# Performance work log

Measured on AMD Instinct MI355X. Metric: run time of the kernel, lower is better.

## Reference

```python
import jax, jax.numpy as jnp
import numpy as np

T, B, D, H = 512, 64, 512, 512

def setup_inputs() -> dict:
    key = jax.random.key(0)
    ks = jax.random.split(key, 12)
    s_in = 1.0 / np.sqrt(D + H)
    s_res = 1.0 / np.sqrt(D)
    inp = {
        'inputs': jax.random.normal(ks[0], (T, B, D), jnp.float32),
        'W_f': jax.random.uniform(ks[1], (H, D + H), jnp.float32, -s_in, s_in),
        'b_f': jax.random.uniform(ks[2], (H,), jnp.float32, -s_in, s_in),
        'W_i': jax.random.uniform(ks[3], (H, D + H), jnp.float32, -s_in, s_in),
        'b_i': jax.random.uniform(ks[4], (H,), jnp.float32, -s_in, s_in),
        'W_g': jax.random.uniform(ks[5], (H, D + H), jnp.float32, -s_in, s_in),
        'b_g': jax.random.uniform(ks[6], (H,), jnp.float32, -s_in, s_in),
        'W_o': jax.random.uniform(ks[7], (H, D + H), jnp.float32, -s_in, s_in),
        'b_o': jax.random.uniform(ks[8], (H,), jnp.float32, -s_in, s_in),
        'W_r': jax.random.uniform(ks[9], (H, D), jnp.float32, -s_res, s_res),
        'b_r': jax.random.uniform(ks[10], (H,), jnp.float32, -s_res, s_res),
    }
    return inp

def reference(inputs, W_f, b_f, W_i, b_i, W_g, b_g, W_o, b_o, W_r, b_r):
    Bsz = inputs.shape[1]
    Hd = W_f.shape[0]
    # residual projection is independent of recurrence: batch it over all timesteps
    res = jnp.einsum('tbd,hd->tbh', inputs, W_r) + b_r  # [T,B,H]

    def step(carry, xr):
        hx, cx = carry
        x, r = xr
        combined = jnp.concatenate([x, hx], axis=1)  # [B, D+H]
        f = jax.nn.sigmoid(combined @ W_f.T + b_f)
        i = jax.nn.sigmoid(combined @ W_i.T + b_i)
        g = jnp.tanh(combined @ W_g.T + b_g)
        o = jax.nn.sigmoid(combined @ W_o.T + b_o)
        cx = f * cx + i * g
        hx = o * jnp.tanh(cx) + r  # use_residual=True
        return (hx, cx), hx

    hx0 = jnp.zeros((Bsz, Hd), inputs.dtype)
    cx0 = jnp.zeros((Bsz, Hd), inputs.dtype)
    (hx, cx), stacked = jax.lax.scan(step, (hx0, cx0), (inputs, res))
    return stacked, (hx, cx)
```

## Files before the change

kernel.cpp:

```cpp
#include <hip/hip_runtime.h>


typedef __bf16         bfrag8 __attribute__((ext_vector_type(8)));
typedef float          f32x4v __attribute__((ext_vector_type(4)));
typedef unsigned short u16x8  __attribute__((ext_vector_type(8)));
typedef int            v4i    __attribute__((ext_vector_type(4)));

#define N_TB    32768
#define GXW     2560
#define OUT_HX  16777216
#define OUT_CX  16809984

__device__ __forceinline__ float bf2f(unsigned short u) {
  unsigned int x = ((unsigned int)u) << 16;
  return __builtin_bit_cast(float, x);
}
__device__ __forceinline__ unsigned short f2bf(float f) {
  unsigned int x = __builtin_bit_cast(unsigned int, f);
  x = x + 0x7FFFu + ((x >> 16) & 1u);
  return (unsigned short)(x >> 16);
}
__device__ __forceinline__ float sigf(float x) {
  x = fminf(fmaxf(x, -30.f), 30.f);
  return 1.f / (1.f + __expf(-x));
}
__device__ __forceinline__ float tanh_f(float x) {
  x = fminf(fmaxf(x, -15.f), 15.f);
  float e = __expf(-2.f * x);
  return (1.f - e) / (1.f + e);
}

__global__ void cvt_kernel(const float* __restrict__ in, unsigned short* __restrict__ out) {
  int i = (blockIdx.x * 256 + threadIdx.x) * 4;
  float4 v = *(const float4*)(in + i);
  ushort4 o = make_ushort4(f2bf(v.x), f2bf(v.y), f2bf(v.z), f2bf(v.w));
  *(ushort4*)(out + i) = o;
}

__global__ void repack_kernel(const float* __restrict__ Wf, const float* __restrict__ Wi,
                              const float* __restrict__ Wg, const float* __restrict__ Wo,
                              const float* __restrict__ Wr,
                              const float* __restrict__ bfp, const float* __restrict__ bip,
                              const float* __restrict__ bgp, const float* __restrict__ bop,
                              const float* __restrict__ brp,
                              unsigned short* __restrict__ Wc, unsigned short* __restrict__ Whx,
                              float* __restrict__ bias) {
  int tid = blockIdx.x * 256 + threadIdx.x;
  if (tid < 262144) {
    int row = tid >> 7;
    int k4  = (tid & 127) * 4;
    int g = row >> 9, h = row & 511;
    const float* W = (g == 0) ? Wf : (g == 1) ? Wi : (g == 2) ? Wg : Wo;
    float4 a = *(const float4*)(W + (size_t)h * 1024 + k4);
    float4 b = *(const float4*)(W + (size_t)h * 1024 + 512 + k4);
    *(ushort4*)(Wc  + (size_t)row * 512 + k4) = make_ushort4(f2bf(a.x), f2bf(a.y), f2bf(a.z), f2bf(a.w));
    *(ushort4*)(Whx + (size_t)row * 512 + k4) = make_ushort4(f2bf(b.x), f2bf(b.y), f2bf(b.z), f2bf(b.w));
  } else if (tid < 327680) {
    int t2 = tid - 262144;
    int row = t2 >> 7;
    int k4  = (t2 & 127) * 4;
    float4 a = *(const float4*)(Wr + (size_t)row * 512 + k4);
    *(ushort4*)(Wc + (size_t)(2048 + row) * 512 + k4) =
        make_ushort4(f2bf(a.x), f2bf(a.y), f2bf(a.z), f2bf(a.w));
  }
  if (tid < 2560) {
    float v;
    if      (tid <  512) v = bfp[tid];
    else if (tid < 1024) v = bip[tid - 512];
    else if (tid < 1536) v = bgp[tid - 1024];
    else if (tid < 2048) v = bop[tid - 1536];
    else                 v = brp[tid - 2048];
    bias[tid] = v;
  }
}

__global__ __launch_bounds__(256)
void gemm_kernel(const unsigned short* __restrict__ A, const unsigned short* __restrict__ B,
                 const float* __restrict__ bias, unsigned short* __restrict__ C) {
  const int bm = blockIdx.x;
  const int bn = blockIdx.y;
  const int tid = threadIdx.x;
  const int lane = tid & 63;
  const int w = tid >> 6;
  const int wm = w & 1, wn = w >> 1;
  const int col = lane & 15, q = lane >> 4;

  __shared__ unsigned short As[128 * 64] __attribute__((aligned(16)));
  __shared__ unsigned short Bs[128 * 64] __attribute__((aligned(16)));

  f32x4v acc[4][4] = {};

  for (int kt = 0; kt < 8; ++kt) {
    __syncthreads();
    #pragma unroll
    for (int p = 0; p < 4; ++p) {
      int idx = p * 256 + tid;
      int row = idx >> 3, gc = idx & 7;
      *(u16x8*)(&As[idx * 8]) = *(const u16x8*)(A + (size_t)(bm * 128 + row) * 512 + kt * 64 + gc * 8);
      *(u16x8*)(&Bs[idx * 8]) = *(const u16x8*)(B + (size_t)(bn * 128 + row) * 512 + kt * 64 + gc * 8);
    }
    __syncthreads();
    #pragma unroll
    for (int kk = 0; kk < 2; ++kk) {
      bfrag8 af[4], bfr[4];
      #pragma unroll
      for (int mt = 0; mt < 4; ++mt)
        af[mt] = *(const bfrag8*)(&As[(wm * 64 + mt * 16 + col) * 64 + kk * 32 + q * 8]);
      #pragma unroll
      for (int nt = 0; nt < 4; ++nt)
        bfr[nt] = *(const bfrag8*)(&Bs[(wn * 64 + nt * 16 + col) * 64 + kk * 32 + q * 8]);
      #pragma unroll
      for (int mt = 0; mt < 4; ++mt)
        #pragma unroll
        for (int nt = 0; nt < 4; ++nt)
          acc[mt][nt] = __builtin_amdgcn_mfma_f32_16x16x32_bf16(af[mt], bfr[nt], acc[mt][nt], 0, 0, 0);
    }
  }
  #pragma unroll
  for (int mt = 0; mt < 4; ++mt) {
    const int m0 = bm * 128 + wm * 64 + mt * 16 + q * 4;
    const float4 b4 = *(const float4*)(bias + m0);
    #pragma unroll
    for (int nt = 0; nt < 4; ++nt) {
      const int n = bn * 128 + wn * 64 + nt * 16 + col;
      f32x4v v = acc[mt][nt];
      ushort4 o = make_ushort4(f2bf(v[0] + b4.x), f2bf(v[1] + b4.y),
                               f2bf(v[2] + b4.z), f2bf(v[3] + b4.w));
      *(ushort4*)(C + (size_t)n * GXW + m0) = o;
    }
  }
}

__global__ __launch_bounds__(256, 1)
void recur_kernel(const unsigned short* __restrict__ Whx, const unsigned short* __restrict__ gx,
                  unsigned short* __restrict__ hbuf, int* flags, float* __restrict__ out) {
  const int jb = blockIdx.x;
  const int tid = threadIdx.x;
  const int lane = tid & 63;
  const int w = tid >> 6;
  const int gp = w & 1;
  const int mh = w >> 1;
  const int col = lane & 15;
  const int q = lane >> 4;

  __shared__ float S[4][64][20] __attribute__((aligned(16)));
  __shared__ unsigned short Hs[64][520] __attribute__((aligned(16)));

  bfrag8 Bf[2][16];
  #pragma unroll
  for (int g2 = 0; g2 < 2; ++g2) {
    const int gate = gp * 2 + g2;
    const unsigned short* wp = Whx + (size_t)(gate * 512 + jb * 16 + col) * 512 + q * 8;
    #pragma unroll
    for (int kk = 0; kk < 16; ++kk)
      Bf[g2][kk] = *(const bfrag8*)(wp + kk * 32);
  }

  const int ub = tid >> 2;
  const int ucg = (tid & 3) * 4;
  float c4[4] = {0.f, 0.f, 0.f, 0.f};

  ushort4 gxv[4], rv;
  {
    const unsigned short* g0 = gx + (size_t)ub * GXW + jb * 16 + ucg;
    #pragma unroll
    for (int gg = 0; gg < 4; ++gg) gxv[gg] = *(const ushort4*)(g0 + gg * 512);
    rv = *(const ushort4*)(g0 + 2048);
  }

  for (int t = 0; t < 512; ++t) {
    if (t > 0) {
      if (tid < 32) {
        while (__hip_atomic_load(flags + tid, __ATOMIC_RELAXED, __HIP_MEMORY_SCOPE_AGENT) < t) {
        }
      }
      __syncthreads();
    }

    {
      const char* hsrc = (const char*)(hbuf + (t & 1) * 32768);
      v4i tmp[16];
      #pragma unroll
      for (int i = 0; i < 16; ++i) {
        const char* p = hsrc + (size_t)(i * 256 + tid) * 16;
        asm volatile("global_load_dwordx4 %0, %1, off sc0 sc1"
                     : "=v"(tmp[i]) : "v"(p) : "memory");
      }
      asm volatile("s_waitcnt vmcnt(0)" ::: "memory");
      #pragma unroll
      for (int i = 0; i < 16; ++i) {
        int idx = i * 256 + tid;
        *(v4i*)((char*)&Hs[0][0] + (size_t)(idx >> 6) * 1040 + (idx & 63) * 16) = tmp[i];
      }
    }
    __syncthreads();

    bfrag8 Af[2][16];
    #pragma unroll
    for (int mt = 0; mt < 2; ++mt) {
      const unsigned short* ap = &Hs[mh * 32 + mt * 16 + col][q * 8];
      #pragma unroll
      for (int kk = 0; kk < 16; ++kk)
        Af[mt][kk] = *(const bfrag8*)(ap + kk * 32);
    }
    f32x4v acc[2][2] = {};
    #pragma unroll
    for (int kk = 0; kk < 16; ++kk)
      #pragma unroll
      for (int mt = 0; mt < 2; ++mt)
        #pragma unroll
        for (int g2 = 0; g2 < 2; ++g2)
          acc[mt][g2] = __builtin_amdgcn_mfma_f32_16x16x32_bf16(Af[mt][kk], Bf[g2][kk], acc[mt][g2], 0, 0, 0);

    #pragma unroll
    for (int mt = 0; mt < 2; ++mt)
      #pragma unroll
      for (int g2 = 0; g2 < 2; ++g2) {
        const int gate = gp * 2 + g2;
        const int b0 = mh * 32 + mt * 16 + q * 4;
        #pragma unroll
        for (int r = 0; r < 4; ++r)
          S[gate][b0 + r][col] = acc[mt][g2][r];
      }
    __syncthreads();

    float pre[4][4];
    #pragma unroll
    for (int gg = 0; gg < 4; ++gg) {
      float4 sv = *(const float4*)&S[gg][ub][ucg];
      pre[gg][0] = sv.x + bf2f(gxv[gg].x);
      pre[gg][1] = sv.y + bf2f(gxv[gg].y);
      pre[gg][2] = sv.z + bf2f(gxv[gg].z);
      pre[gg][3] = sv.w + bf2f(gxv[gg].w);
    }
    float rres[4] = {bf2f(rv.x), bf2f(rv.y), bf2f(rv.z), bf2f(rv.w)};
    float hv[4];
    #pragma unroll
    for (int j = 0; j < 4; ++j) {
      float fg = sigf(pre[0][j]);
      float ig = sigf(pre[1][j]);
      float gg = tanh_f(pre[2][j]);
      float og = sigf(pre[3][j]);
      c4[j] = fg * c4[j] + ig * gg;
      hv[j] = og * tanh_f(c4[j]) + rres[j];
    }
    float4 h4 = make_float4(hv[0], hv[1], hv[2], hv[3]);

    if (t < 511) {
      ushort4 hb4 = make_ushort4(f2bf(hv[0]), f2bf(hv[1]), f2bf(hv[2]), f2bf(hv[3]));
      union { ushort4 u4; unsigned long long u64; } pk;
      pk.u4 = hb4;
      __hip_atomic_store((unsigned long long*)(hbuf + ((t + 1) & 1) * 32768 + ub * 512 + jb * 16 + ucg),
                         pk.u64, __ATOMIC_RELAXED, __HIP_MEMORY_SCOPE_AGENT);
      asm volatile("s_waitcnt vmcnt(0)" ::: "memory");
      __syncthreads();
      if (tid == 0)
        __hip_atomic_store(flags + jb, t + 1, __ATOMIC_RELAXED, __HIP_MEMORY_SCOPE_AGENT);
    }

    *(float4*)(out + (size_t)t * 32768 + ub * 512 + jb * 16 + ucg) = h4;

    if (t == 511) {
      *(float4*)(out + OUT_HX + ub * 512 + jb * 16 + ucg) = h4;
      *(float4*)(out + OUT_CX + ub * 512 + jb * 16 + ucg) = make_float4(c4[0], c4[1], c4[2], c4[3]);
    } else {
      const unsigned short* gn = gx + (size_t)((t + 1) * 64 + ub) * GXW + jb * 16 + ucg;
      #pragma unroll
      for (int gg = 0; gg < 4; ++gg) gxv[gg] = *(const ushort4*)(gn + gg * 512);
      rv = *(const ushort4*)(gn + 2048);
    }
  }
}

extern "C" void kernel_launch(void* const* d_in, const int* in_sizes, int n_in,
                              void* d_out, int out_size, void* d_ws, size_t ws_size,
                              hipStream_t stream) {
  const float* inputs = (const float*)d_in[0];
  const float* Wf = (const float*)d_in[1];
  const float* bf_ = (const float*)d_in[2];
  const float* Wi = (const float*)d_in[3];
  const float* bi_ = (const float*)d_in[4];
  const float* Wg = (const float*)d_in[5];
  const float* bg_ = (const float*)d_in[6];
  const float* Wo = (const float*)d_in[7];
  const float* bo_ = (const float*)d_in[8];
  const float* Wr = (const float*)d_in[9];
  const float* br_ = (const float*)d_in[10];
  float* out = (float*)d_out;

  unsigned short* X    = (unsigned short*)d_ws;
  unsigned short* Wc   = X + 16777216;
  unsigned short* Whx  = Wc + 1310720;
  float*          bias = (float*)(Whx + 1048576);
  unsigned short* gx   = (unsigned short*)(bias + 2560);
  unsigned short* hbuf = gx + 83886080;
  int*            flags = (int*)(hbuf + 65536);
  const size_t ws_needed = 206186624;
  if (ws_size < ws_needed) return;

  hipMemsetAsync(hbuf, 0, 65536 * 2 + 32 * 4, stream);

  cvt_kernel<<<16384, 256, 0, stream>>>(inputs, X);
  repack_kernel<<<1280, 256, 0, stream>>>(Wf, Wi, Wg, Wo, Wr, bf_, bi_, bg_, bo_, br_,
                                          Wc, Whx, bias);
  gemm_kernel<<<dim3(20, 256), 256, 0, stream>>>(Wc, X, bias, gx);
  recur_kernel<<<32, 256, 0, stream>>>(Whx, gx, hbuf, flags, out);
}
```

Baseline: 2.498 ms.

## Replace flag-based grid sync with per-element tagged h buffer and 512 threads

```diff
diff --git a/kernel.cpp b/kernel.cpp
--- a/kernel.cpp
+++ b/kernel.cpp
@@ -5,6 +5,7 @@
 typedef float          f32x4v __attribute__((ext_vector_type(4)));
 typedef unsigned short u16x8  __attribute__((ext_vector_type(8)));
 typedef int            v4i    __attribute__((ext_vector_type(4)));
+typedef int            v2i    __attribute__((ext_vector_type(2)));
 
 #define N_TB    32768
 #define GXW     2560
@@ -131,9 +132,9 @@
   }
 }
 
-__global__ __launch_bounds__(256, 1)
+__global__ __launch_bounds__(512, 1)
 void recur_kernel(const unsigned short* __restrict__ Whx, const unsigned short* __restrict__ gx,
-                  unsigned short* __restrict__ hbuf, int* flags, float* __restrict__ out) {
+                  unsigned int* __restrict__ hbufF, float* __restrict__ out) {
   const int jb = blockIdx.x;
   const int tid = threadIdx.x;
   const int lane = tid & 63;
@@ -156,118 +157,119 @@
       Bf[g2][kk] = *(const bfrag8*)(wp + kk * 32);
   }
 
-  const int ub = tid >> 2;
-  const int ucg = (tid & 3) * 4;
-  float c4[4] = {0.f, 0.f, 0.f, 0.f};
-
-  ushort4 gxv[4], rv;
+  const int ub = tid >> 3;
+  const int uc = (tid & 7) * 2;
+
+  float c2[2] = {0.f, 0.f};
+
+  ushort2 gxv[4], rv;
   {
-    const unsigned short* g0 = gx + (size_t)ub * GXW + jb * 16 + ucg;
-    #pragma unroll
-    for (int gg = 0; gg < 4; ++gg) gxv[gg] = *(const ushort4*)(g0 + gg * 512);
-    rv = *(const ushort4*)(g0 + 2048);
+    const unsigned short* g0 = gx + (size_t)ub * GXW + jb * 16 + uc;
+    #pragma unroll
+    for (int gg = 0; gg < 4; ++gg) gxv[gg] = *(const ushort2*)(g0 + gg * 512);
+    rv = *(const ushort2*)(g0 + 2048);
   }
 
   for (int t = 0; t < 512; ++t) {
-    if (t > 0) {
-      if (tid < 32) {
-        while (__hip_atomic_load(flags + tid, __ATOMIC_RELAXED, __HIP_MEMORY_SCOPE_AGENT) < t) {
+    {
+      const char* hs = (const char*)(hbufF + (t & 1) * 32768);
+      v4i ta[8], tb_[8];
+      const int need = (t > 0);
+      for (;;) {
+        #pragma unroll
+        for (int i = 0; i < 8; ++i) {
+          const char* p = hs + (size_t)(i * 512 + tid) * 32;
+          asm volatile("global_load_dwordx4 %0, %1, off sc0 sc1"
+                       : "=v"(ta[i]) : "v"(p) : "memory");
+          asm volatile("global_load_dwordx4 %0, %1, off sc0 sc1"
+                       : "=v"(tb_[i]) : "v"(p + 16) : "memory");
         }
+        asm volatile("s_waitcnt vmcnt(0)" ::: "memory");
+        if (!need) break;
+        unsigned int bad = 0;
+        #pragma unroll
+        for (int i = 0; i < 8; ++i)
+          #pragma unroll
+          for (int j = 0; j < 4; ++j) {
+            bad |= (unsigned int)(ta[i][j]  ^ t) & 0xFFFFu;
+            bad |= (unsigned int)(tb_[i][j] ^ t) & 0xFFFFu;
+          }
+        if (!bad) break;
       }
-      __syncthreads();
-    }
-
+      #pragma unroll
+      for (int i = 0; i < 8; ++i) {
+        const int u = i * 512 + tid;
+        v4i o;
+        o[0] = (int)(((unsigned int)ta[i][0]  >> 16) | ((unsigned int)ta[i][1]  & 0xFFFF0000u));
+        o[1] = (int)(((unsigned int)ta[i][2]  >> 16) | ((unsigned int)ta[i][3]  & 0xFFFF0000u));
+        o[2] = (int)(((unsigned int)tb_[i][0] >> 16) | ((unsigned int)tb_[i][1] & 0xFFFF0000u));
+        o[3] = (int)(((unsigned int)tb_[i][2] >> 16) | ((unsigned int)tb_[i][3] & 0xFFFF0000u));
+        *(v4i*)((char*)&Hs[0][0] + (size_t)(u >> 6) * 1040 + (u & 63) * 16) = o;
+      }
+    }
+    __syncthreads();
+
+    bfrag8 Af[16];
     {
-      const char* hsrc = (const char*)(hbuf + (t & 1) * 32768);
-      v4i tmp[16];
-      #pragma unroll
-      for (int i = 0; i < 16; ++i) {
-        const char* p = hsrc + (size_t)(i * 256 + tid) * 16;
-        asm volatile("global_load_dwordx4 %0, %1, off sc0 sc1"
-                     : "=v"(tmp[i]) : "v"(p) : "memory");
-      }
-      asm volatile("s_waitcnt vmcnt(0)" ::: "memory");
-      #pragma unroll
-      for (int i = 0; i < 16; ++i) {
-        int idx = i * 256 + tid;
-        *(v4i*)((char*)&Hs[0][0] + (size_t)(idx >> 6) * 1040 + (idx & 63) * 16) = tmp[i];
-      }
+      const unsigned short* ap = &Hs[mh * 16 + col][q * 8];
+      #pragma unroll
+      for (int kk = 0; kk < 16; ++kk)
+        Af[kk] = *(const bfrag8*)(ap + kk * 32);
+    }
+    f32x4v acc[2] = {};
+    #pragma unroll
+    for (int kk = 0; kk < 16; ++kk) {
+      acc[0] = __builtin_amdgcn_mfma_f32_16x16x32_bf16(Af[kk], Bf[0][kk], acc[0], 0, 0, 0);
+      acc[1] = __builtin_amdgcn_mfma_f32_16x16x32_bf16(Af[kk], Bf[1][kk], acc[1], 0, 0, 0);
+    }
+    #pragma unroll
+    for (int g2 = 0; g2 < 2; ++g2) {
+      const int gate = gp * 2 + g2;
+      const int b0 = mh * 16 + q * 4;
+      #pragma unroll
+      for (int r = 0; r < 4; ++r)
+        S[gate][b0 + r][col] = acc[g2][r];
     }
     __syncthreads();
 
-    bfrag8 Af[2][16];
-    #pragma unroll
-    for (int mt = 0; mt < 2; ++mt) {
-      const unsigned short* ap = &Hs[mh * 32 + mt * 16 + col][q * 8];
-      #pragma unroll
-      for (int kk = 0; kk < 16; ++kk)
-        Af[mt][kk] = *(const bfrag8*)(ap + kk * 32);
-    }
-    f32x4v acc[2][2] = {};
-    #pragma unroll
-    for (int kk = 0; kk < 16; ++kk)
-      #pragma unroll
-      for (int mt = 0; mt < 2; ++mt)
-        #pragma unroll
-        for (int g2 = 0; g2 < 2; ++g2)
-          acc[mt][g2] = __builtin_amdgcn_mfma_f32_16x16x32_bf16(Af[mt][kk], Bf[g2][kk], acc[mt][g2], 0, 0, 0);
-
-    #pragma unroll
-    for (int mt = 0; mt < 2; ++mt)
-      #pragma unroll
-      for (int g2 = 0; g2 < 2; ++g2) {
-        const int gate = gp * 2 + g2;
-        const int b0 = mh * 32 + mt * 16 + q * 4;
-        #pragma unroll
-        for (int r = 0; r < 4; ++r)
-          S[gate][b0 + r][col] = acc[mt][g2][r];
-      }
-    __syncthreads();
-
-    float pre[4][4];
+    float pre[4][2];
     #pragma unroll
     for (int gg = 0; gg < 4; ++gg) {
-      float4 sv = *(const float4*)&S[gg][ub][ucg];
+      float2 sv = *(const float2*)&S[gg][ub][uc];
       pre[gg][0] = sv.x + bf2f(gxv[gg].x);
       pre[gg][1] = sv.y + bf2f(gxv[gg].y);
-      pre[gg][2] = sv.z + bf2f(gxv[gg].z);
-      pre[gg][3] = sv.w + bf2f(gxv[gg].w);
-    }
-    float rres[4] = {bf2f(rv.x), bf2f(rv.y), bf2f(rv.z), bf2f(rv.w)};
-    float hv[4];
-    #pragma unroll
-    for (int j = 0; j < 4; ++j) {
+    }
+    float rres[2] = {bf2f(rv.x), bf2f(rv.y)};
+    float hv[2];
+    #pragma unroll
+    for (int j = 0; j < 2; ++j) {
       float fg = sigf(pre[0][j]);
       float ig = sigf(pre[1][j]);
       float gg = tanh_f(pre[2][j]);
       float og = sigf(pre[3][j]);
-      c4[j] = fg * c4[j] + ig * gg;
-      hv[j] = og * tanh_f(c4[j]) + rres[j];
-    }
-    float4 h4 = make_float4(hv[0], hv[1], hv[2], hv[3]);
+      c2[j] = fg * c2[j] + ig * gg;
+      hv[j] = og * tanh_f(c2[j]) + rres[j];
+    }
 
     if (t < 511) {
-      ushort4 hb4 = make_ushort4(f2bf(hv[0]), f2bf(hv[1]), f2bf(hv[2]), f2bf(hv[3]));
-      union { ushort4 u4; unsigned long long u64; } pk;
-      pk.u4 = hb4;
-      __hip_atomic_store((unsigned long long*)(hbuf + ((t + 1) & 1) * 32768 + ub * 512 + jb * 16 + ucg),
-                         pk.u64, __ATOMIC_RELAXED, __HIP_MEMORY_SCOPE_AGENT);
-      asm volatile("s_waitcnt vmcnt(0)" ::: "memory");
-      __syncthreads();
-      if (tid == 0)
-        __hip_atomic_store(flags + jb, t + 1, __ATOMIC_RELAXED, __HIP_MEMORY_SCOPE_AGENT);
-    }
-
-    *(float4*)(out + (size_t)t * 32768 + ub * 512 + jb * 16 + ucg) = h4;
+      v2i pk;
+      pk[0] = (int)(((unsigned int)f2bf(hv[0]) << 16) | (unsigned int)(t + 1));
+      pk[1] = (int)(((unsigned int)f2bf(hv[1]) << 16) | (unsigned int)(t + 1));
+      unsigned int* dst = hbufF + ((t + 1) & 1) * 32768 + ub * 512 + jb * 16 + uc;
+      asm volatile("global_store_dwordx2 %0, %1, off sc0 sc1"
+                   :: "v"(dst), "v"(pk) : "memory");
+    }
+
+    *(float2*)(out + (size_t)t * 32768 + ub * 512 + jb * 16 + uc) = make_float2(hv[0], hv[1]);
 
     if (t == 511) {
-      *(float4*)(out + OUT_HX + ub * 512 + jb * 16 + ucg) = h4;
-      *(float4*)(out + OUT_CX + ub * 512 + jb * 16 + ucg) = make_float4(c4[0], c4[1], c4[2], c4[3]);
+      *(float2*)(out + OUT_HX + ub * 512 + jb * 16 + uc) = make_float2(hv[0], hv[1]);
+      *(float2*)(out + OUT_CX + ub * 512 + jb * 16 + uc) = make_float2(c2[0], c2[1]);
     } else {
-      const unsigned short* gn = gx + (size_t)((t + 1) * 64 + ub) * GXW + jb * 16 + ucg;
-      #pragma unroll
-      for (int gg = 0; gg < 4; ++gg) gxv[gg] = *(const ushort4*)(gn + gg * 512);
-      rv = *(const ushort4*)(gn + 2048);
+      const unsigned short* gn = gx + (size_t)((t + 1) * 64 + ub) * GXW + jb * 16 + uc;
+      #pragma unroll
+      for (int gg = 0; gg < 4; ++gg) gxv[gg] = *(const ushort2*)(gn + gg * 512);
+      rv = *(const ushort2*)(gn + 2048);
     }
   }
 }
@@ -293,16 +295,14 @@
   unsigned short* Whx  = Wc + 1310720;
   float*          bias = (float*)(Whx + 1048576);
   unsigned short* gx   = (unsigned short*)(bias + 2560);
-  unsigned short* hbuf = gx + 83886080;
-  int*            flags = (int*)(hbuf + 65536);
-  const size_t ws_needed = 206186624;
+  unsigned int*   hbufF = (unsigned int*)d_ws;
+  const size_t ws_needed = 206055424;
   if (ws_size < ws_needed) return;
-
-  hipMemsetAsync(hbuf, 0, 65536 * 2 + 32 * 4, stream);
 
   cvt_kernel<<<16384, 256, 0, stream>>>(inputs, X);
   repack_kernel<<<1280, 256, 0, stream>>>(Wf, Wi, Wg, Wo, Wr, bf_, bi_, bg_, bo_, br_,
                                           Wc, Whx, bias);
   gemm_kernel<<<dim3(20, 256), 256, 0, stream>>>(Wc, X, bias, gx);
-  recur_kernel<<<32, 256, 0, stream>>>(Whx, gx, hbuf, flags, out);
-}
+  hipMemsetAsync(hbufF, 0, 2 * 32768 * 4, stream);
+  recur_kernel<<<32, 512, 0, stream>>>(Whx, gx, hbufF, out);
+}
```

Result: slower. 2.690 ms (+7.7%).
